# Performance work log

Hardware: AMD Instinct MI355X
Metric: run time of the kernel (lower is better)

Reference implementation:

```python
import jax, jax.numpy as jnp
import numpy as np

D_MODEL = 2048
N_HEADS = 16
D_K = D_MODEL // N_HEADS
BATCH = 4
SEQ = 2048


def setup_inputs() -> dict:
    key = jax.random.key(0)
    ks = jax.random.split(key, 9)
    s = 1.0 / np.sqrt(D_MODEL)
    return {
        "x": jax.random.normal(ks[0], (BATCH, SEQ, D_MODEL), dtype=jnp.float32),
        "wq_w": jax.random.normal(ks[1], (D_MODEL, D_MODEL), dtype=jnp.float32) * s,
        "wq_b": jax.random.normal(ks[2], (D_MODEL,), dtype=jnp.float32) * 0.02,
        "wk_w": jax.random.normal(ks[3], (D_MODEL, D_MODEL), dtype=jnp.float32) * s,
        "wk_b": jax.random.normal(ks[4], (D_MODEL,), dtype=jnp.float32) * 0.02,
        "wv_w": jax.random.normal(ks[5], (D_MODEL, D_MODEL), dtype=jnp.float32) * s,
        "wv_b": jax.random.normal(ks[6], (D_MODEL,), dtype=jnp.float32) * 0.02,
        "wo_w": jax.random.normal(ks[7], (D_MODEL, D_MODEL), dtype=jnp.float32) * s,
        "wo_b": jax.random.normal(ks[8], (D_MODEL,), dtype=jnp.float32) * 0.02,
    }


def reference(x, wq_w, wq_b, wk_w, wk_b, wv_w, wv_b, wo_w, wo_b):
    b, s, _ = x.shape
    # Linear projections (torch Linear: x @ W^T + b)
    def split_heads(t):  # (b, s, d_model) -> (b, h, s, d_k)
        return t.reshape(b, s, N_HEADS, D_K).transpose(0, 2, 1, 3)
    q = split_heads(x @ wq_w.T + wq_b)
    k = split_heads(x @ wk_w.T + wk_b)
    v = split_heads(x @ wv_w.T + wv_b)
    scale = 1.0 / jnp.sqrt(jnp.asarray(D_K, dtype=x.dtype))
    scores = jnp.einsum("bhqd,bhkd->bhqk", q, k) * scale  # (b, h, s, s)
    attn = jax.nn.softmax(scores, axis=-1)
    ctx = jnp.einsum("bhqk,bhkd->bhqd", attn, v)
    ctx = ctx.transpose(0, 2, 1, 3).reshape(b, s, D_MODEL)
    out = ctx @ wo_w.T + wo_b
    return out
```

## Files before the change

### kernel.cpp

```cpp
#include <hip/hip_runtime.h>
#include <hip/hip_bf16.h>
#include <math.h>

typedef __attribute__((ext_vector_type(8))) short short8;
typedef __attribute__((ext_vector_type(4))) float f32x4;
typedef __attribute__((ext_vector_type(16))) float f32x16;
typedef __attribute__((ext_vector_type(4))) unsigned short u16x4;
typedef __attribute__((ext_vector_type(8))) unsigned short u16x8;
typedef __attribute__((ext_vector_type(4))) unsigned int u32x4;
typedef __attribute__((ext_vector_type(2))) int i32x2;
typedef unsigned short u16;
typedef unsigned int u32;

#define DM 2048
#define SQ 2048
#define NB 4
#define NH 16
#define DKH 128
#define KT 64
#define NT (SQ / KT)

__device__ __forceinline__ u16 f2bf(float f) {
  unsigned u = __float_as_uint(f);
  u += 0x7fffu + ((u >> 16) & 1u);
  return (u16)(u >> 16);
}

__device__ __forceinline__ u32 cvtpk(float lo, float hi) {
  u32 r;
  asm("v_cvt_pk_bf16_f32 %0, %1, %2" : "=v"(r) : "v"(lo), "v"(hi));
  return r;
}

__device__ __forceinline__ void gload16(const u16* g, u16* lds) {
  __builtin_amdgcn_global_load_lds(
      (const __attribute__((address_space(1))) unsigned int*)g,
      (__attribute__((address_space(3))) unsigned int*)lds, 16, 0, 0);
}

__global__ void cvt_bf16(const float* __restrict__ in, u16* __restrict__ out, int n) {
  int i = (blockIdx.x * blockDim.x + threadIdx.x) * 4;
  if (i >= n) return;
  float4 v = *(const float4*)(in + i);
  u16x4 o;
  o.x = f2bf(v.x); o.y = f2bf(v.y); o.z = f2bf(v.z); o.w = f2bf(v.w);
  *(u16x4*)(out + i) = o;
}

__global__ void cvt_w4(const float* __restrict__ w0, const float* __restrict__ w1,
                       const float* __restrict__ w2, const float* __restrict__ w3,
                       u16* __restrict__ dst) {
  const int sel = blockIdx.y;
  const float* src;
  switch (sel) {
    case 0: src = w0; break;
    case 1: src = w1; break;
    case 2: src = w2; break;
    default: src = w3; break;
  }
  const int i = (blockIdx.x * blockDim.x + threadIdx.x) * 4;
  float4 v = *(const float4*)(src + i);
  u16x4 o;
  o.x = f2bf(v.x); o.y = f2bf(v.y); o.z = f2bf(v.z); o.w = f2bf(v.w);
  *(u16x4*)(dst + (size_t)sel * DM * DM + i) = o;
}


#define STG_A(T, HALF)                                                \
  do {                                                                \
    u16* d_ = &smA[((T) & 1) * 16384 + (((HALF) * 128 + w * 16) << 6)]; \
    const u16* s_ = As + (size_t)((HALF) * 128) * K + (size_t)(T) * 64; \
    gload16(s_, d_);                                                  \
    gload16(s_ + (size_t)8 * K, d_ + 8 * 64);                         \
  } while (0)

#define STG_B(T, HALF)                                                \
  do {                                                                \
    u16* d_ = &smB[((T) & 1) * 16384 + (((HALF) * 128 + w * 16) << 6)]; \
    const u16* s_ = Bs + (size_t)((HALF) * 128) * K + (size_t)(T) * 64; \
    gload16(s_, d_);                                                  \
    gload16(s_ + (size_t)8 * K, d_ + 8 * 64);                         \
  } while (0)

#define LDA(QM)                                                          \
  do {                                                                   \
    const u16* p_ = &smA[bi * 16384 + ((wr * 128 + (QM) * 64 + c5) << 6)]; \
    _Pragma("unroll") for (int s = 0; s < 4; ++s) {                      \
      const int sl_ = (((s << 1) | hi) ^ (c5 & 7)) << 3;                 \
      af[0][s] = *(const short8*)&p_[sl_];                               \
      af[1][s] = *(const short8*)&p_[32 * 64 + sl_];                     \
    }                                                                    \
  } while (0)

#define LDB(QN)                                                          \
  do {                                                                   \
    const u16* p_ = &smB[bi * 16384 + ((wc * 64 + (QN) * 32 + c5) << 6)]; \
    _Pragma("unroll") for (int s = 0; s < 4; ++s)                        \
      bf[QN][s] = *(const short8*)&p_[(((s << 1) | hi) ^ (c5 & 7)) << 3]; \
  } while (0)

#define MFMA_Q(QM, QN)                                                             \
  __builtin_amdgcn_s_setprio(1);                                                   \
  _Pragma("unroll") for (int s = 0; s < 4; ++s) {                                  \
    acc[(QM) * 2][(QN)] = __builtin_amdgcn_mfma_f32_32x32x16_bf16(                 \
        af[0][s], bf[QN][s], acc[(QM) * 2][(QN)], 0, 0, 0);                        \
    acc[(QM) * 2 + 1][(QN)] = __builtin_amdgcn_mfma_f32_32x32x16_bf16(             \
        af[1][s], bf[QN][s], acc[(QM) * 2 + 1][(QN)], 0, 0, 0);                    \
  }                                                                                \
  __builtin_amdgcn_s_setprio(0);

#define WAIT_LGKM                                         \
  asm volatile("s_waitcnt lgkmcnt(0)" ::: "memory");      \
  __builtin_amdgcn_sched_barrier(0);

template <bool OUTF32>
__global__ __launch_bounds__(512, 2) void gemm8p(
    const u16* __restrict__ A, const u16* __restrict__ B,
    const float* __restrict__ bias, void* __restrict__ Cout,
    int M, int N, int K, float oscale) {
  __shared__ u16 smA[2 * 16384];
  __shared__ u16 smB[2 * 16384];
  const int tid = threadIdx.x;
  const int w = tid >> 6, l = tid & 63;
  const int c5 = l & 31, hi = l >> 5;
  const int wr = w >> 2, wc = w & 3;

  int flat = blockIdx.x + (int)gridDim.x * (int)blockIdx.y;
  const int nwg = (int)(gridDim.x * gridDim.y);
  flat = (flat & 7) * (nwg >> 3) + (flat >> 3);
  const int m0 = (flat / (int)gridDim.x) * 256, n0 = (flat % (int)gridDim.x) * 256;

  const int NSTEP = K / 64;
  f32x16 acc[4][2] = {};

  const int sgrp = l >> 3;
  const int scol = ((l & 7) ^ sgrp) * 8;
  const u16* As = A + (size_t)(m0 + w * 16 + sgrp) * K + scol;
  const u16* Bs = B + (size_t)(n0 + w * 16 + sgrp) * K + scol;

  STG_A(0, 0); STG_A(0, 1); STG_B(0, 0); STG_B(0, 1);
  STG_B(1, 0); STG_A(1, 0);
  asm volatile("s_waitcnt vmcnt(4)" ::: "memory");
  __builtin_amdgcn_s_barrier();

  short8 af[2][4], bf[2][4];
  for (int t = 0; t < NSTEP; ++t) {
    const int bi = t & 1;
    LDA(0); LDB(0);
    if (t + 1 < NSTEP) STG_B(t + 1, 1);
    __builtin_amdgcn_s_barrier();
    WAIT_LGKM;
    MFMA_Q(0, 0);
    __builtin_amdgcn_s_barrier();
    LDB(1);
    if (t + 1 < NSTEP) STG_A(t + 1, 1);
    __builtin_amdgcn_s_barrier();
    WAIT_LGKM;
    MFMA_Q(0, 1);
    __builtin_amdgcn_s_barrier();
    LDA(1);
    if (t + 2 < NSTEP) STG_B(t + 2, 0);
    __builtin_amdgcn_s_barrier();
    WAIT_LGKM;
    MFMA_Q(1, 1);
    __builtin_amdgcn_s_barrier();
    if (t + 2 < NSTEP) STG_A(t + 2, 0);
    __builtin_amdgcn_s_barrier();
    MFMA_Q(1, 0);
    if (t + 2 < NSTEP)
      asm volatile("s_waitcnt vmcnt(4)" ::: "memory");
    else if (t + 1 < NSTEP)
      asm volatile("s_waitcnt vmcnt(0)" ::: "memory");
    __builtin_amdgcn_s_barrier();
  }

#pragma unroll
  for (int nf = 0; nf < 2; ++nf) {
    const int col = n0 + wc * 64 + nf * 32 + c5;
    const float bv = bias[col];
#pragma unroll
    for (int mf = 0; mf < 4; ++mf) {
#pragma unroll
      for (int r = 0; r < 16; ++r) {
        const int row = m0 + wr * 128 + mf * 32 + (r & 3) + 8 * (r >> 2) + 4 * hi;
        const float v = (acc[mf][nf][r] + bv) * oscale;
        if (OUTF32)
          ((float*)Cout)[(size_t)row * N + col] = v;
        else
          ((u16*)Cout)[(size_t)row * N + col] = f2bf(v);
      }
    }
  }
}

__global__ __launch_bounds__(512, 2) void attn(
    const u16* __restrict__ Q, const u16* __restrict__ K,
    const u16* __restrict__ V, u16* __restrict__ O) {
  __shared__ u16 smK[2 * 8192];
  __shared__ u16 smV[2 * 9216];
  __shared__ float alScr[8 * 32];

  const int tid = threadIdx.x;
  const int w = tid >> 6, l = tid & 63;
  const int c5 = l & 31, hi = l >> 5;

  int flat = blockIdx.x + ((int)blockIdx.y << 3) + ((int)blockIdx.z << 7);
  flat = (flat & 7) * 64 + (flat >> 3);
  const int qt = flat & 7, h = (flat >> 3) & 15, b = flat >> 7;

  const int q0 = qt * 256 + w * 32;
  const size_t rowb = (size_t)b * SQ;
  const int hoff = h * DKH;

  short8 qf[8];
#pragma unroll
  for (int ds = 0; ds < 8; ++ds)
    qf[ds] = *(const short8*)&Q[(rowb + q0 + c5) * DM + hoff + ds * 16 + hi * 8];

  f32x16 o[4] = {};
  float mrow = -1e30f, lsum = 0.f;

  const int vdg = tid >> 5;
  const int kvp = (tid & 31) * 2;
  u16x8 va, vb;

  {
    const u16* vp = &V[(rowb + kvp) * DM + hoff + vdg * 8];
    va = *(const u16x8*)vp;
    vb = *(const u16x8*)(vp + DM);
#pragma unroll
    for (int uu = 0; uu < 2; ++uu) {
      const int u = w * 2 + uu;
      const int row = u * 4 + (l >> 4);
      const int col16 = (l & 15) ^ (row & 15);
      gload16(&K[(rowb + row) * DM + hoff + col16 * 8], &smK[u * 512]);
    }
#pragma unroll
    for (int i = 0; i < 8; ++i) {
      const int d = vdg * 8 + i;
      *(u32*)&smV[d * 72 + kvp] = (u32)va[i] | ((u32)vb[i] << 16);
    }
  }
  __syncthreads();

  int buf = 0;
  for (int t = 0; t < NT; ++t) {
    const int nb = buf ^ 1;
    if (t + 1 < NT) {
      const size_t kvr = rowb + (size_t)(t + 1) * KT;
      const u16* vp = &V[(kvr + kvp) * DM + hoff + vdg * 8];
      va = *(const u16x8*)vp;
      vb = *(const u16x8*)(vp + DM);
#pragma unroll
      for (int uu = 0; uu < 2; ++uu) {
        const int u = w * 2 + uu;
        const int row = u * 4 + (l >> 4);
        const int col16 = (l & 15) ^ (row & 15);
        gload16(&K[(kvr + row) * DM + hoff + col16 * 8], &smK[nb * 8192 + u * 512]);
      }
    }

    f32x16 s[2] = {};
    __builtin_amdgcn_s_setprio(1);
#pragma unroll
    for (int ni = 0; ni < 2; ++ni) {
      const int row = ni * 32 + c5;
#pragma unroll
      for (int ds = 0; ds < 8; ++ds) {
        const short8 kf = *(const short8*)&smK[buf * 8192 + row * 128 + (((ds << 1) | hi) ^ (row & 15)) * 8];
        s[ni] = __builtin_amdgcn_mfma_f32_32x32x16_bf16(kf, qf[ds], s[ni], 0, 0, 0);
      }
    }
    __builtin_amdgcn_s_setprio(0);

    float mx = s[0][0];
#pragma unroll
    for (int ni = 0; ni < 2; ++ni)
#pragma unroll
      for (int i = 0; i < 16; ++i)
        mx = fmaxf(mx, s[ni][i]);
    i32x2 sw = __builtin_amdgcn_permlane32_swap(__float_as_int(mx), __float_as_int(mx), false, false);
    const float gmax = fmaxf(__int_as_float(sw.x), __int_as_float(sw.y));

    if (__any(gmax > mrow + 10.0f)) {
      const float mn = fmaxf(mrow, gmax);
      const float al = exp2f(mrow - mn);
      mrow = mn;
      lsum *= al;
      alScr[w * 32 + c5] = al;
#pragma unroll
      for (int r = 0; r < 16; ++r) {
        const float av = alScr[w * 32 + (r & 3) + 8 * (r >> 2) + 4 * hi];
#pragma unroll
        for (int dg = 0; dg < 4; ++dg) o[dg][r] *= av;
      }
    }

    float ps0 = 0.f, ps1 = 0.f;
#pragma unroll
    for (int i = 0; i < 16; ++i) {
      const float p0 = exp2f(s[0][i] - mrow);
      const float p1 = exp2f(s[1][i] - mrow);
      s[0][i] = p0; s[1][i] = p1;
      ps0 += p0; ps1 += p1;
    }
    lsum += ps0 + ps1;

    __builtin_amdgcn_s_setprio(1);
#pragma unroll
    for (int ks = 0; ks < 4; ++ks) {
      const int b0 = (ks & 1) * 8;
      const int ni = ks >> 1;
      const u32 A0 = cvtpk(s[ni][b0 + 0], s[ni][b0 + 1]);
      const u32 A1 = cvtpk(s[ni][b0 + 4], s[ni][b0 + 5]);
      const u32 B0 = cvtpk(s[ni][b0 + 2], s[ni][b0 + 3]);
      const u32 B1 = cvtpk(s[ni][b0 + 6], s[ni][b0 + 7]);
      const i32x2 r0 = __builtin_amdgcn_permlane32_swap((int)A0, (int)A1, false, false);
      const i32x2 r1 = __builtin_amdgcn_permlane32_swap((int)B0, (int)B1, false, false);
      u32x4 paw;
      paw.x = (u32)r0.x; paw.y = (u32)r1.x; paw.z = (u32)r0.y; paw.w = (u32)r1.y;
      const short8 pa = *(const short8*)&paw;
#pragma unroll
      for (int dg = 0; dg < 4; ++dg) {
        const int rowd = dg * 32 + c5;
        const short8 vf = *(const short8*)&smV[buf * 9216 + rowd * 72 + ks * 16 + hi * 8];
        o[dg] = __builtin_amdgcn_mfma_f32_32x32x16_bf16(pa, vf, o[dg], 0, 0, 0);
      }
    }
    __builtin_amdgcn_s_setprio(0);

    if (t + 1 < NT) {
#pragma unroll
      for (int i = 0; i < 8; ++i) {
        const int d = vdg * 8 + i;
        *(u32*)&smV[nb * 9216 + d * 72 + kvp] = (u32)va[i] | ((u32)vb[i] << 16);
      }
    }
    __syncthreads();
    buf = nb;
  }

  {
    const i32x2 sl = __builtin_amdgcn_permlane32_swap(__float_as_int(lsum), __float_as_int(lsum), false, false);
    const float tot = __int_as_float(sl.x) + __int_as_float(sl.y);
    alScr[w * 32 + c5] = 1.0f / tot;
  }
#pragma unroll
  for (int r = 0; r < 16; ++r) {
    const int qloc = (r & 3) + 8 * (r >> 2) + 4 * hi;
    const float inv = alScr[w * 32 + qloc];
    const size_t orow = (rowb + q0 + qloc) * DM + hoff;
#pragma unroll
    for (int dg = 0; dg < 4; ++dg)
      O[orow + dg * 32 + c5] = f2bf(o[dg][r] * inv);
  }
}

extern "C" void kernel_launch(void* const* d_in, const int* in_sizes, int n_in,
                              void* d_out, int out_size, void* d_ws, size_t ws_size,
                              hipStream_t stream) {
  const float* x    = (const float*)d_in[0];
  const float* wq_w = (const float*)d_in[1];
  const float* wq_b = (const float*)d_in[2];
  const float* wk_w = (const float*)d_in[3];
  const float* wk_b = (const float*)d_in[4];
  const float* wv_w = (const float*)d_in[5];
  const float* wv_b = (const float*)d_in[6];
  const float* wo_w = (const float*)d_in[7];
  const float* wo_b = (const float*)d_in[8];
  float* out = (float*)d_out;

  u16* p = (u16*)d_ws;
  u16* xb  = p; p += (size_t)NB * SQ * DM;
  u16* wqb = p; p += (size_t)DM * DM;
  u16* wkb = p; p += (size_t)DM * DM;
  u16* wvb = p; p += (size_t)DM * DM;
  u16* wob = p; p += (size_t)DM * DM;
  u16* Qb  = p; p += (size_t)NB * SQ * DM;
  u16* Kb  = p; p += (size_t)NB * SQ * DM;
  u16* Vb  = p; p += (size_t)NB * SQ * DM;
  u16* ctx = xb;

  const int nx = NB * SQ * DM;
  cvt_bf16<<<dim3(nx / 1024), dim3(256), 0, stream>>>(x, xb, nx);
  cvt_w4<<<dim3(DM * DM / 1024, 4), dim3(256), 0, stream>>>(wq_w, wk_w, wv_w, wo_w, wqb);

  const float sc2 = 0.08838834764831845f * 1.4426950408889634f;
  dim3 gg(DM / 256, (NB * SQ) / 256);
  gemm8p<false><<<gg, dim3(512), 0, stream>>>(xb, wqb, wq_b, Qb, NB * SQ, DM, DM, sc2);
  gemm8p<false><<<gg, dim3(512), 0, stream>>>(xb, wkb, wk_b, Kb, NB * SQ, DM, DM, 1.0f);
  gemm8p<false><<<gg, dim3(512), 0, stream>>>(xb, wvb, wv_b, Vb, NB * SQ, DM, DM, 1.0f);

  attn<<<dim3(SQ / 256, NH, NB), dim3(512), 0, stream>>>(Qb, Kb, Vb, ctx);

  gemm8p<true><<<gg, dim3(512), 0, stream>>>(ctx, wob, wo_b, out, NB * SQ, DM, DM, 1.0f);
}
```

Before: 563.6 us.

## Fuse Q/K/V projections into one GEMM with interleaved QKV output

Merges the three separate Q, K and V projection GEMMs into a single launch over concatenated weights (N = 3*DM). The output is written as one interleaved QKV buffer that attention reads with stride 3*DM, and per-column bias and scale are selected by segment. This removes two launches and improves grid fill. Attention also drops the V double-buffer in shared memory and adds an extra barrier per tile, which lowers LDS use but serializes the V store against the PV MFMAs.

```diff
diff --git a/kernel.cpp b/kernel.cpp
--- a/kernel.cpp
+++ b/kernel.cpp
@@ -19,6 +19,8 @@
 #define DKH 128
 #define KT 64
 #define NT (SQ / KT)
+#define LD3 (3 * DM)
+#define QSCALE (0.08838834764831845f * 1.4426950408889634f)
 
 __device__ __forceinline__ u16 f2bf(float f) {
   unsigned u = __float_as_uint(f);
@@ -113,11 +115,12 @@
   asm volatile("s_waitcnt lgkmcnt(0)" ::: "memory");      \
   __builtin_amdgcn_sched_barrier(0);
 
-template <bool OUTF32>
+template <int MODE>
 __global__ __launch_bounds__(512, 2) void gemm8p(
     const u16* __restrict__ A, const u16* __restrict__ B,
-    const float* __restrict__ bias, void* __restrict__ Cout,
-    int M, int N, int K, float oscale) {
+    const float* __restrict__ bq, const float* __restrict__ bk,
+    const float* __restrict__ bvp, void* __restrict__ Cout,
+    int M, int N, int K) {
   __shared__ u16 smA[2 * 16384];
   __shared__ u16 smB[2 * 16384];
   const int tid = threadIdx.x;
@@ -177,14 +180,23 @@
 #pragma unroll
   for (int nf = 0; nf < 2; ++nf) {
     const int col = n0 + wc * 64 + nf * 32 + c5;
-    const float bv = bias[col];
+    float bval, os;
+    if (MODE == 0) {
+      const int seg = col >> 11;
+      const float* bp = seg == 0 ? bq : (seg == 1 ? bk : bvp);
+      bval = bp[col & (DM - 1)];
+      os = (seg == 0) ? QSCALE : 1.0f;
+    } else {
+      bval = bq[col];
+      os = 1.0f;
+    }
 #pragma unroll
     for (int mf = 0; mf < 4; ++mf) {
 #pragma unroll
       for (int r = 0; r < 16; ++r) {
         const int row = m0 + wr * 128 + mf * 32 + (r & 3) + 8 * (r >> 2) + 4 * hi;
-        const float v = (acc[mf][nf][r] + bv) * oscale;
-        if (OUTF32)
+        const float v = (acc[mf][nf][r] + bval) * os;
+        if (MODE == 1)
           ((float*)Cout)[(size_t)row * N + col] = v;
         else
           ((u16*)Cout)[(size_t)row * N + col] = f2bf(v);
@@ -194,11 +206,14 @@
 }
 
 __global__ __launch_bounds__(512, 2) void attn(
-    const u16* __restrict__ Q, const u16* __restrict__ K,
-    const u16* __restrict__ V, u16* __restrict__ O) {
+    const u16* __restrict__ QKV, u16* __restrict__ O) {
   __shared__ u16 smK[2 * 8192];
-  __shared__ u16 smV[2 * 9216];
+  __shared__ u16 smV[9216];
   __shared__ float alScr[8 * 32];
+
+  const u16* Qp = QKV;
+  const u16* Kp = QKV + DM;
+  const u16* Vp = QKV + 2 * DM;
 
   const int tid = threadIdx.x;
   const int w = tid >> 6, l = tid & 63;
@@ -215,7 +230,7 @@
   short8 qf[8];
 #pragma unroll
   for (int ds = 0; ds < 8; ++ds)
-    qf[ds] = *(const short8*)&Q[(rowb + q0 + c5) * DM + hoff + ds * 16 + hi * 8];
+    qf[ds] = *(const short8*)&Qp[(rowb + q0 + c5) * LD3 + hoff + ds * 16 + hi * 8];
 
   f32x16 o[4] = {};
   float mrow = -1e30f, lsum = 0.f;
@@ -225,16 +240,16 @@
   u16x8 va, vb;
 
   {
-    const u16* vp = &V[(rowb + kvp) * DM + hoff + vdg * 8];
-    va = *(const u16x8*)vp;
-    vb = *(const u16x8*)(vp + DM);
 #pragma unroll
     for (int uu = 0; uu < 2; ++uu) {
       const int u = w * 2 + uu;
       const int row = u * 4 + (l >> 4);
       const int col16 = (l & 15) ^ (row & 15);
-      gload16(&K[(rowb + row) * DM + hoff + col16 * 8], &smK[u * 512]);
-    }
+      gload16(&Kp[(rowb + row) * LD3 + hoff + col16 * 8], &smK[u * 512]);
+    }
+    const u16* vp = &Vp[(rowb + kvp) * LD3 + hoff + vdg * 8];
+    va = *(const u16x8*)vp;
+    vb = *(const u16x8*)(vp + LD3);
 #pragma unroll
     for (int i = 0; i < 8; ++i) {
       const int d = vdg * 8 + i;
@@ -248,16 +263,16 @@
     const int nb = buf ^ 1;
     if (t + 1 < NT) {
       const size_t kvr = rowb + (size_t)(t + 1) * KT;
-      const u16* vp = &V[(kvr + kvp) * DM + hoff + vdg * 8];
-      va = *(const u16x8*)vp;
-      vb = *(const u16x8*)(vp + DM);
 #pragma unroll
       for (int uu = 0; uu < 2; ++uu) {
         const int u = w * 2 + uu;
         const int row = u * 4 + (l >> 4);
         const int col16 = (l & 15) ^ (row & 15);
-        gload16(&K[(kvr + row) * DM + hoff + col16 * 8], &smK[nb * 8192 + u * 512]);
-      }
+        gload16(&Kp[(kvr + row) * LD3 + hoff + col16 * 8], &smK[nb * 8192 + u * 512]);
+      }
+      const u16* vp = &Vp[(kvr + kvp) * LD3 + hoff + vdg * 8];
+      va = *(const u16x8*)vp;
+      vb = *(const u16x8*)(vp + LD3);
     }
 
     f32x16 s[2] = {};
@@ -323,20 +338,21 @@
 #pragma unroll
       for (int dg = 0; dg < 4; ++dg) {
         const int rowd = dg * 32 + c5;
-        const short8 vf = *(const short8*)&smV[buf * 9216 + rowd * 72 + ks * 16 + hi * 8];
+        const short8 vf = *(const short8*)&smV[rowd * 72 + ks * 16 + hi * 8];
         o[dg] = __builtin_amdgcn_mfma_f32_32x32x16_bf16(pa, vf, o[dg], 0, 0, 0);
       }
     }
     __builtin_amdgcn_s_setprio(0);
 
+    __syncthreads();
     if (t + 1 < NT) {
 #pragma unroll
       for (int i = 0; i < 8; ++i) {
         const int d = vdg * 8 + i;
-        *(u32*)&smV[nb * 9216 + d * 72 + kvp] = (u32)va[i] | ((u32)vb[i] << 16);
-      }
-    }
-    __syncthreads();
+        *(u32*)&smV[d * 72 + kvp] = (u32)va[i] | ((u32)vb[i] << 16);
+      }
+      __syncthreads();
+    }
     buf = nb;
   }
 
@@ -372,26 +388,22 @@
 
   u16* p = (u16*)d_ws;
   u16* xb  = p; p += (size_t)NB * SQ * DM;
-  u16* wqb = p; p += (size_t)DM * DM;
-  u16* wkb = p; p += (size_t)DM * DM;
-  u16* wvb = p; p += (size_t)DM * DM;
+  u16* wqb = p; p += (size_t)3 * DM * DM;
   u16* wob = p; p += (size_t)DM * DM;
-  u16* Qb  = p; p += (size_t)NB * SQ * DM;
-  u16* Kb  = p; p += (size_t)NB * SQ * DM;
-  u16* Vb  = p; p += (size_t)NB * SQ * DM;
+  u16* QKV = p; p += (size_t)NB * SQ * 3 * DM;
   u16* ctx = xb;
 
   const int nx = NB * SQ * DM;
   cvt_bf16<<<dim3(nx / 1024), dim3(256), 0, stream>>>(x, xb, nx);
   cvt_w4<<<dim3(DM * DM / 1024, 4), dim3(256), 0, stream>>>(wq_w, wk_w, wv_w, wo_w, wqb);
 
-  const float sc2 = 0.08838834764831845f * 1.4426950408889634f;
-  dim3 gg(DM / 256, (NB * SQ) / 256);
-  gemm8p<false><<<gg, dim3(512), 0, stream>>>(xb, wqb, wq_b, Qb, NB * SQ, DM, DM, sc2);
-  gemm8p<false><<<gg, dim3(512), 0, stream>>>(xb, wkb, wk_b, Kb, NB * SQ, DM, DM, 1.0f);
-  gemm8p<false><<<gg, dim3(512), 0, stream>>>(xb, wvb, wv_b, Vb, NB * SQ, DM, DM, 1.0f);
-
-  attn<<<dim3(SQ / 256, NH, NB), dim3(512), 0, stream>>>(Qb, Kb, Vb, ctx);
-
-  gemm8p<true><<<gg, dim3(512), 0, stream>>>(ctx, wob, wo_b, out, NB * SQ, DM, DM, 1.0f);
-}
+  dim3 gg3(3 * DM / 256, (NB * SQ) / 256);
+  gemm8p<0><<<gg3, dim3(512), 0, stream>>>(xb, wqb, wq_b, wk_b, wv_b, QKV,
+                                           NB * SQ, 3 * DM, DM);
+
+  attn<<<dim3(SQ / 256, NH, NB), dim3(512), 0, stream>>>(QKV, ctx);
+
+  dim3 ggo(DM / 256, (NB * SQ) / 256);
+  gemm8p<1><<<ggo, dim3(512), 0, stream>>>(ctx, wob, wo_b, nullptr, nullptr, out,
+                                           NB * SQ, DM, DM);
+}
```

Result: faster. 550.0 us (-2.4%).
